# Performance work log

Hardware: AMD Instinct MI355X
Metric: run time of the kernel (lower is better)

Reference implementation:

```python
import jax, jax.numpy as jnp
import numpy as np

LN_EPS = 1e-5   # torch nn.LayerNorm default
EPS = 1e-3      # module eps for norm denominator


def setup_inputs() -> dict:
    key = jax.random.key(0)
    ks = jax.random.split(key, 4)
    N_msa, N_tok, c_m, c_h, c_z = 64, 384, 64, 32, 128
    m = jax.random.normal(ks[0], (N_msa, N_tok, c_m), dtype=jnp.float32)
    mask = jnp.ones((N_msa, N_tok), dtype=jnp.float32)
    ln_w = jnp.ones((c_m,), dtype=jnp.float32)
    ln_b = jnp.zeros((c_m,), dtype=jnp.float32)
    w1 = jax.random.normal(ks[1], (c_h, c_m), dtype=jnp.float32) * (1.0 / np.sqrt(c_m))
    w2 = jax.random.normal(ks[2], (c_h, c_m), dtype=jnp.float32) * (1.0 / np.sqrt(c_m))
    w_out = jax.random.normal(ks[3], (c_z, c_h * c_h), dtype=jnp.float32) * (1.0 / np.sqrt(c_h * c_h))
    b_out = jnp.zeros((c_z,), dtype=jnp.float32)
    return {"m": m, "mask": mask, "ln_w": ln_w, "ln_b": ln_b,
            "w1": w1, "w2": w2, "w_out": w_out, "b_out": b_out}


def reference(m, mask, ln_w, ln_b, w1, w2, w_out, b_out):
    # LayerNorm over c_m
    mu = jnp.mean(m, axis=-1, keepdims=True)
    var = jnp.var(m, axis=-1, keepdims=True)
    m_n = (m - mu) * jax.lax.rsqrt(var + LN_EPS) * ln_w + ln_b

    maskx = mask[..., None]                                   # (N_msa, N_tok, 1)
    # norm[i,j] = sum_s mask[s,i]*mask[s,j], shape (N_tok, N_tok, 1)
    norm = jnp.einsum('sic,sjc->ijc', maskx, maskx)

    a = jnp.einsum('sim,cm->sic', m_n, w1) * maskx            # (N_msa, N_tok, C)
    b = jnp.einsum('sim,cm->sic', m_n, w2) * maskx            # (N_msa, N_tok, C)

    # mean-of-outer-products over MSA rows: (N_tok, N_tok, C, C)
    outer = jnp.einsum('sic,sjd->ijcd', a, b)
    N_tok, C = a.shape[1], a.shape[2]
    outer = outer.reshape(N_tok, N_tok, C * C)

    out = jnp.einsum('ijk,zk->ijz', outer, w_out) + b_out      # (N_tok, N_tok, c_z)
    return out / (norm + EPS)
```

## Files before the change

### kernel.cpp

```cpp
#include <hip/hip_runtime.h>
#include <stdint.h>

#define NS 64
#define NT 384
#define CM 64
#define CH 32
#define CZ 128

typedef __attribute__((ext_vector_type(8))) short bf16x8;
typedef __attribute__((ext_vector_type(16))) float f32x16;
typedef __attribute__((ext_vector_type(4))) float f32x4;
typedef __attribute__((ext_vector_type(4))) uint32_t u32x4;

#define MFMA __builtin_amdgcn_mfma_f32_32x32x16_bf16

static __device__ __forceinline__ uint16_t f2bf(float f) {
  uint32_t u = __float_as_uint(f);
  u = (u + 0x7FFFu + ((u >> 16) & 1u)) >> 16;
  return (uint16_t)u;
}
static __device__ __forceinline__ uint32_t pack2(float lo, float hi) {
  return (uint32_t)f2bf(lo) | ((uint32_t)f2bf(hi) << 16);
}
static __device__ __forceinline__ int swzO(int x) {
  return x ^ ((((x >> 8) ^ (x >> 11)) & 7) << 4);
}

__global__ __launch_bounds__(256) void k_pre(
    const float* __restrict__ m, const float* __restrict__ mask,
    const float* __restrict__ lnw, const float* __restrict__ lnb,
    const float* __restrict__ w1, const float* __restrict__ w2,
    const float* __restrict__ wout,
    uint16_t* __restrict__ AF2, uint16_t* __restrict__ BF,
    uint16_t* __restrict__ W2, float* __restrict__ invn) {
  __shared__ float4 wsh4[2][1024];
  __shared__ float4 mn4[64 * 17];
  const int b = blockIdx.x;
  const int tid = threadIdx.x;
  if (b < NT) {
    const int i = b;
    const int wv = tid >> 6, lane = tid & 63;
    for (int t = tid; t < 1024; t += 256) {
      wsh4[0][t] = ((const float4*)w1)[t];
      wsh4[1][t] = ((const float4*)w2)[t];
    }
    const float lw = lnw[lane], lb = lnb[lane];
    float* mnf = (float*)mn4;
    for (int s = wv; s < NS; s += 4) {
      float x = m[(s * NT + i) * CM + lane];
      float sum = x, sq = x * x;
#pragma unroll
      for (int off = 32; off; off >>= 1) {
        sum += __shfl_xor(sum, off);
        sq += __shfl_xor(sq, off);
      }
      float mu = sum * (1.f / 64.f);
      float var = sq * (1.f / 64.f) - mu * mu;
      float rs = 1.f / sqrtf(var + 1e-5f);
      mnf[s * 68 + lane] = (x - mu) * rs * lw + lb;
    }
    __syncthreads();
    const int s = lane;
    const int cb = tid >> 6;
    float accA[8] = {0, 0, 0, 0, 0, 0, 0, 0};
    float accB[8] = {0, 0, 0, 0, 0, 0, 0, 0};
#pragma unroll
    for (int q = 0; q < 16; ++q) {
      float4 v = mn4[s * 17 + q];
#pragma unroll
      for (int k = 0; k < 8; ++k) {
        float4 wa = wsh4[0][(cb * 8 + k) * 16 + q];
        float4 wb = wsh4[1][(cb * 8 + k) * 16 + q];
        accA[k] = fmaf(v.x, wa.x, fmaf(v.y, wa.y, fmaf(v.z, wa.z, fmaf(v.w, wa.w, accA[k]))));
        accB[k] = fmaf(v.x, wb.x, fmaf(v.y, wb.y, fmaf(v.z, wb.z, fmaf(v.w, wb.w, accB[k]))));
      }
    }
    const float msk = mask[s * NT + i];
    const int kkq = s >> 4, hh = (s >> 3) & 1, e = s & 7;
    const size_t baseB = ((size_t)(i * 4 + kkq) * 64 + hh * 32) * 8 + e;
#pragma unroll
    for (int k = 0; k < 8; ++k) {
      int c = cb * 8 + k;
      BF[baseB + (size_t)c * 8] = f2bf(accB[k] * msk);
      int rb = (c >> 2) * 48 + (i >> 3);
      int r = (i & 7) * 4 + (c & 3);
      AF2[((size_t)(rb * 4 + kkq) * 64 + hh * 32 + r) * 8 + e] = f2bf(accA[k] * msk);
    }
  } else if (b < NT + 64) {
    const int g = (b - NT) * 256 + tid;
    const int l = g & 63, zt = (g >> 6) & 3, kk = g >> 8;
    const float* src = wout + (zt * 32 + (l & 31)) * 1024 + kk * 16 + (l >> 5) * 8;
    uint16_t* dst = W2 + (size_t)g * 8;
#pragma unroll
    for (int e2 = 0; e2 < 8; ++e2) dst[e2] = f2bf(src[e2]);
  } else {
    const int t = (b - NT - 64) * 256 + tid;
    const int i = t / NT, j = t - i * NT;
    float acc = 0.f;
#pragma unroll 8
    for (int s2 = 0; s2 < NS; ++s2) acc += mask[s2 * NT + i] * mask[s2 * NT + j];
    invn[t] = 1.f / (acc + 1e-3f);
  }
}

__global__ __launch_bounds__(512, 2) void k_main(
    const uint16_t* __restrict__ AF2, const uint16_t* __restrict__ BF,
    const uint16_t* __restrict__ W2, const float* __restrict__ b_out,
    const float* __restrict__ invn, float* __restrict__ out) {
  extern __shared__ char lds[];
  const int tid = threadIdx.x;
  const int wv = tid >> 6, l = tid & 63;
  const int lo5 = l & 31, hi = l >> 5;
  const int i0 = blockIdx.x * 16, j0 = blockIdx.y * 8;
  const int ib0 = blockIdx.x * 2;
  const int jt = wv;
  const int kh = wv >> 2, mp = (wv >> 1) & 1, zp = wv & 1;

  bf16x8 bfr[4];
  {
    const uint16_t* p = BF + (size_t)(j0 + jt) * 4 * 512 + (size_t)l * 8;
#pragma unroll
    for (int kk = 0; kk < 4; ++kk) bfr[kk] = *(const bf16x8*)(p + kk * 512);
  }

  f32x16 acc2[2][2];
#pragma unroll
  for (int mi = 0; mi < 2; ++mi)
#pragma unroll
    for (int zi = 0; zi < 2; ++zi) acc2[mi][zi] = (f32x16){};

  for (int cbk = 0; cbk < 8; ++cbk) {
    const int cur = cbk & 1;
    char* ldsO = lds + cur * 32768;
    char* ldsW = lds + 65536 + cur * 32768;

    u32x4 wst[4];
    {
      const uint32_t* src = (const uint32_t*)(W2 + (size_t)cbk * 16384);
#pragma unroll
      for (int it = 0; it < 4; ++it) wst[it] = *(const u32x4*)(src + it * 2048 + tid * 4);
    }

    f32x16 acc1[2];
    acc1[0] = (f32x16){};
    acc1[1] = (f32x16){};
    {
      const uint16_t* Ap = AF2 + (size_t)(cbk * 48 + ib0) * 4 * 512 + (size_t)l * 8;
#pragma unroll
      for (int kk = 0; kk < 4; ++kk) {
        bf16x8 a0 = *(const bf16x8*)(Ap + kk * 512);
        bf16x8 a1 = *(const bf16x8*)(Ap + (4 + kk) * 512);
        acc1[0] = MFMA(bfr[kk], a0, acc1[0], 0, 0, 0);
        acc1[1] = MFMA(bfr[kk], a1, acc1[1], 0, 0, 0);
      }
    }
#pragma unroll
    for (int it = 0; it < 4; ++it) *(u32x4*)(ldsW + it * 8192 + tid * 16) = wst[it];
#pragma unroll
    for (int h = 0; h < 2; ++h) {
      const int p = (h * 8 + (lo5 >> 2)) * 8 + jt;
      const int base = p * 256 + (lo5 & 3) * 64 + hi * 8;
#pragma unroll
      for (int g = 0; g < 4; ++g) {
        uint64_t v = (uint64_t)pack2(acc1[h][4 * g + 0], acc1[h][4 * g + 1]) |
                     ((uint64_t)pack2(acc1[h][4 * g + 2], acc1[h][4 * g + 3]) << 32);
        *(uint64_t*)(ldsO + swzO(base + g * 16)) = v;
      }
    }
    __syncthreads();

#pragma unroll
    for (int kx = 0; kx < 4; ++kx) {
      const int kkl = kh * 4 + kx;
      bf16x8 of[2], wf[2];
#pragma unroll
      for (int mi = 0; mi < 2; ++mi) {
        const int mt = mp * 2 + mi;
        of[mi] = *(const bf16x8*)(ldsO + swzO((mt * 32 + lo5) * 256 + kkl * 32 + hi * 16));
      }
#pragma unroll
      for (int zi = 0; zi < 2; ++zi) {
        const int zt = zp * 2 + zi;
        wf[zi] = *(const bf16x8*)(ldsW + (kkl * 4 + zt) * 1024 + l * 16);
      }
#pragma unroll
      for (int mi = 0; mi < 2; ++mi)
#pragma unroll
        for (int zi = 0; zi < 2; ++zi)
          acc2[mi][zi] = MFMA(of[mi], wf[zi], acc2[mi][zi], 0, 0, 0);
    }
  }

  const int sidx = mp * 2 + zp;
  const int wbase = (sidx < 2) ? sidx * 16384 : 65536 + (sidx - 2) * 16384;
  if (kh == 1) {
#pragma unroll
    for (int mi = 0; mi < 2; ++mi)
#pragma unroll
      for (int zi = 0; zi < 2; ++zi)
#pragma unroll
        for (int g = 0; g < 4; ++g) {
          f32x4 v = {acc2[mi][zi][4 * g + 0], acc2[mi][zi][4 * g + 1],
                     acc2[mi][zi][4 * g + 2], acc2[mi][zi][4 * g + 3]};
          *(f32x4*)(lds + wbase + ((mi * 2 + zi) * 4 + g) * 1024 + l * 16) = v;
        }
  }
  __syncthreads();
  if (kh == 0) {
#pragma unroll
    for (int mi = 0; mi < 2; ++mi)
#pragma unroll
      for (int zi = 0; zi < 2; ++zi)
#pragma unroll
        for (int g = 0; g < 4; ++g) {
          f32x4 v = *(const f32x4*)(lds + wbase + ((mi * 2 + zi) * 4 + g) * 1024 + l * 16);
#pragma unroll
          for (int jj = 0; jj < 4; ++jj) acc2[mi][zi][4 * g + jj] += v[jj];
        }
  }
  if (tid < 128)
    ((float*)(lds + 98304))[tid] = invn[(size_t)(i0 + (tid >> 3)) * NT + j0 + (tid & 7)];
  __syncthreads();
  if (kh == 0) {
    const float bo0 = b_out[(zp * 2) * 32 + lo5];
    const float bo1 = b_out[(zp * 2 + 1) * 32 + lo5];
    const float* invl = (const float*)(lds + 98304);
#pragma unroll
    for (int mi = 0; mi < 2; ++mi) {
      const int mt = mp * 2 + mi;
#pragma unroll
      for (int e = 0; e < 16; ++e) {
        const int row = mt * 32 + (e & 3) + 8 * (e >> 2) + 4 * hi;
        const float inv = invl[row];
        const size_t n = (size_t)(i0 + (row >> 3)) * NT + j0 + (row & 7);
        out[n * CZ + zp * 64 + lo5] = (acc2[mi][0][e] + bo0) * inv;
        out[n * CZ + zp * 64 + 32 + lo5] = (acc2[mi][1][e] + bo1) * inv;
      }
    }
  }
}

extern "C" void kernel_launch(void* const* d_in, const int* in_sizes, int n_in,
                              void* d_out, int out_size, void* d_ws, size_t ws_size,
                              hipStream_t stream) {
  const float* m    = (const float*)d_in[0];
  const float* mask = (const float*)d_in[1];
  const float* lnw  = (const float*)d_in[2];
  const float* lnb  = (const float*)d_in[3];
  const float* w1   = (const float*)d_in[4];
  const float* w2   = (const float*)d_in[5];
  const float* wout = (const float*)d_in[6];
  const float* bout = (const float*)d_in[7];
  float* out = (float*)d_out;

  char* ws = (char*)d_ws;
  uint16_t* AF2 = (uint16_t*)ws;
  uint16_t* BF  = (uint16_t*)(ws + 1572864);
  uint16_t* W2  = (uint16_t*)(ws + 3145728);
  float* invn   = (float*)(ws + 3407872);

  k_pre<<<1024, 256, 0, stream>>>(m, mask, lnw, lnb, w1, w2, wout, AF2, BF, W2, invn);

  (void)hipFuncSetAttribute(reinterpret_cast<const void*>(k_main),
                            hipFuncAttributeMaxDynamicSharedMemorySize, 131072);
  k_main<<<dim3(NT / 16, NT / 8), 512, 131072, stream>>>(AF2, BF, W2, bout, invn, out);
}
```

Measured before the change: 195.1 us.

## Halve k_main tile, read W_out fragments from global, drop split-K reduction

Each block of k_main now covers 8x8 token pairs instead of 16x8, which doubles the grid. The W_out fragments are loaded straight from global/L2 into registers rather than staged through LDS. Each wave owns a full K range for one 32x32 output tile, which removes the cross-wave split-K reduction through LDS. LDS drops to about 33KB static, launch bounds target 4 blocks per CU, and the first-stage product is software-pipelined with one barrier per step. The trade is more repeated global reads of W_out and of the B fragments across the larger grid, in exchange for higher occupancy and less LDS traffic.

```diff
diff --git a/kernel.cpp b/kernel.cpp
--- a/kernel.cpp
+++ b/kernel.cpp
@@ -9,8 +9,6 @@
 
 typedef __attribute__((ext_vector_type(8))) short bf16x8;
 typedef __attribute__((ext_vector_type(16))) float f32x16;
-typedef __attribute__((ext_vector_type(4))) float f32x4;
-typedef __attribute__((ext_vector_type(4))) uint32_t u32x4;
 
 #define MFMA __builtin_amdgcn_mfma_f32_32x32x16_bf16
 
@@ -103,18 +101,21 @@
   }
 }
 
-__global__ __launch_bounds__(512, 2) void k_main(
+__global__ __launch_bounds__(512, 4) void k_main(
     const uint16_t* __restrict__ AF2, const uint16_t* __restrict__ BF,
     const uint16_t* __restrict__ W2, const float* __restrict__ b_out,
     const float* __restrict__ invn, float* __restrict__ out) {
-  extern __shared__ char lds[];
+  __shared__ __align__(16) char lds[2 * 16384 + 256];
+  float* invLds = (float*)(lds + 32768);
   const int tid = threadIdx.x;
   const int wv = tid >> 6, l = tid & 63;
   const int lo5 = l & 31, hi = l >> 5;
-  const int i0 = blockIdx.x * 16, j0 = blockIdx.y * 8;
-  const int ib0 = blockIdx.x * 2;
+  const int ib = blockIdx.x;
+  const int i0 = blockIdx.x * 8, j0 = blockIdx.y * 8;
   const int jt = wv;
-  const int kh = wv >> 2, mp = (wv >> 1) & 1, zp = wv & 1;
+  const int mp = wv >> 2, zp = wv & 3;
+
+  if (tid < 64) invLds[tid] = invn[(size_t)(i0 + (tid >> 3)) * NT + j0 + (tid & 7)];
 
   bf16x8 bfr[4];
   {
@@ -123,120 +124,73 @@
     for (int kk = 0; kk < 4; ++kk) bfr[kk] = *(const bf16x8*)(p + kk * 512);
   }
 
-  f32x16 acc2[2][2];
-#pragma unroll
-  for (int mi = 0; mi < 2; ++mi)
-#pragma unroll
-    for (int zi = 0; zi < 2; ++zi) acc2[mi][zi] = (f32x16){};
-
-  for (int cbk = 0; cbk < 8; ++cbk) {
-    const int cur = cbk & 1;
-    char* ldsO = lds + cur * 32768;
-    char* ldsW = lds + 65536 + cur * 32768;
-
-    u32x4 wst[4];
+  f32x16 acc2 = (f32x16){};
+
+
+  {
+    const uint16_t* Ap = AF2 + ((size_t)(0 * 48 + ib) * 4) * 512 + (size_t)l * 8;
+    f32x16 acc1 = (f32x16){};
+#pragma unroll
+    for (int kk = 0; kk < 4; ++kk) {
+      bf16x8 afr = *(const bf16x8*)(Ap + kk * 512);
+      acc1 = MFMA(bfr[kk], afr, acc1, 0, 0, 0);
+    }
+    const int p = (lo5 >> 2) * 8 + jt;
+    const int base = p * 256 + (lo5 & 3) * 64 + hi * 8;
+#pragma unroll
+    for (int g = 0; g < 4; ++g) {
+      uint64_t v = (uint64_t)pack2(acc1[4 * g + 0], acc1[4 * g + 1]) |
+                   ((uint64_t)pack2(acc1[4 * g + 2], acc1[4 * g + 3]) << 32);
+      *(uint64_t*)(lds + swzO(base + g * 16)) = v;
+    }
+  }
+  __syncthreads();
+
+  const int p2base = (mp * 32 + lo5) * 256 + hi * 16;
+
+  for (int cbk = 1; cbk <= 8; ++cbk) {
+    f32x16 acc1 = (f32x16){};
+    if (cbk < 8) {
+      const uint16_t* Ap = AF2 + ((size_t)(cbk * 48 + ib) * 4) * 512 + (size_t)l * 8;
+#pragma unroll
+      for (int kk = 0; kk < 4; ++kk) {
+        bf16x8 afr = *(const bf16x8*)(Ap + kk * 512);
+        acc1 = MFMA(bfr[kk], afr, acc1, 0, 0, 0);
+      }
+    }
+
     {
-      const uint32_t* src = (const uint32_t*)(W2 + (size_t)cbk * 16384);
-#pragma unroll
-      for (int it = 0; it < 4; ++it) wst[it] = *(const u32x4*)(src + it * 2048 + tid * 4);
-    }
-
-    f32x16 acc1[2];
-    acc1[0] = (f32x16){};
-    acc1[1] = (f32x16){};
-    {
-      const uint16_t* Ap = AF2 + (size_t)(cbk * 48 + ib0) * 4 * 512 + (size_t)l * 8;
-#pragma unroll
-      for (int kk = 0; kk < 4; ++kk) {
-        bf16x8 a0 = *(const bf16x8*)(Ap + kk * 512);
-        bf16x8 a1 = *(const bf16x8*)(Ap + (4 + kk) * 512);
-        acc1[0] = MFMA(bfr[kk], a0, acc1[0], 0, 0, 0);
-        acc1[1] = MFMA(bfr[kk], a1, acc1[1], 0, 0, 0);
-      }
-    }
-#pragma unroll
-    for (int it = 0; it < 4; ++it) *(u32x4*)(ldsW + it * 8192 + tid * 16) = wst[it];
-#pragma unroll
-    for (int h = 0; h < 2; ++h) {
-      const int p = (h * 8 + (lo5 >> 2)) * 8 + jt;
+      char* ldsO = lds + ((cbk - 1) & 1) * 16384;
+      const uint16_t* Wp = W2 + ((size_t)(((cbk - 1) * 8) * 4 + zp) * 64 + l) * 8;
+#pragma unroll
+      for (int kx = 0; kx < 8; ++kx) {
+        bf16x8 of = *(const bf16x8*)(ldsO + swzO(p2base + kx * 32));
+        bf16x8 wf = *(const bf16x8*)(Wp + (size_t)kx * 4 * 512);
+        acc2 = MFMA(of, wf, acc2, 0, 0, 0);
+      }
+    }
+
+    if (cbk < 8) {
+      char* ldsO = lds + (cbk & 1) * 16384;
+      const int p = (lo5 >> 2) * 8 + jt;
       const int base = p * 256 + (lo5 & 3) * 64 + hi * 8;
 #pragma unroll
       for (int g = 0; g < 4; ++g) {
-        uint64_t v = (uint64_t)pack2(acc1[h][4 * g + 0], acc1[h][4 * g + 1]) |
-                     ((uint64_t)pack2(acc1[h][4 * g + 2], acc1[h][4 * g + 3]) << 32);
+        uint64_t v = (uint64_t)pack2(acc1[4 * g + 0], acc1[4 * g + 1]) |
+                     ((uint64_t)pack2(acc1[4 * g + 2], acc1[4 * g + 3]) << 32);
         *(uint64_t*)(ldsO + swzO(base + g * 16)) = v;
       }
-    }
-    __syncthreads();
-
-#pragma unroll
-    for (int kx = 0; kx < 4; ++kx) {
-      const int kkl = kh * 4 + kx;
-      bf16x8 of[2], wf[2];
-#pragma unroll
-      for (int mi = 0; mi < 2; ++mi) {
-        const int mt = mp * 2 + mi;
-        of[mi] = *(const bf16x8*)(ldsO + swzO((mt * 32 + lo5) * 256 + kkl * 32 + hi * 16));
-      }
-#pragma unroll
-      for (int zi = 0; zi < 2; ++zi) {
-        const int zt = zp * 2 + zi;
-        wf[zi] = *(const bf16x8*)(ldsW + (kkl * 4 + zt) * 1024 + l * 16);
-      }
-#pragma unroll
-      for (int mi = 0; mi < 2; ++mi)
-#pragma unroll
-        for (int zi = 0; zi < 2; ++zi)
-          acc2[mi][zi] = MFMA(of[mi], wf[zi], acc2[mi][zi], 0, 0, 0);
-    }
-  }
-
-  const int sidx = mp * 2 + zp;
-  const int wbase = (sidx < 2) ? sidx * 16384 : 65536 + (sidx - 2) * 16384;
-  if (kh == 1) {
-#pragma unroll
-    for (int mi = 0; mi < 2; ++mi)
-#pragma unroll
-      for (int zi = 0; zi < 2; ++zi)
-#pragma unroll
-        for (int g = 0; g < 4; ++g) {
-          f32x4 v = {acc2[mi][zi][4 * g + 0], acc2[mi][zi][4 * g + 1],
-                     acc2[mi][zi][4 * g + 2], acc2[mi][zi][4 * g + 3]};
-          *(f32x4*)(lds + wbase + ((mi * 2 + zi) * 4 + g) * 1024 + l * 16) = v;
-        }
-  }
-  __syncthreads();
-  if (kh == 0) {
-#pragma unroll
-    for (int mi = 0; mi < 2; ++mi)
-#pragma unroll
-      for (int zi = 0; zi < 2; ++zi)
-#pragma unroll
-        for (int g = 0; g < 4; ++g) {
-          f32x4 v = *(const f32x4*)(lds + wbase + ((mi * 2 + zi) * 4 + g) * 1024 + l * 16);
-#pragma unroll
-          for (int jj = 0; jj < 4; ++jj) acc2[mi][zi][4 * g + jj] += v[jj];
-        }
-  }
-  if (tid < 128)
-    ((float*)(lds + 98304))[tid] = invn[(size_t)(i0 + (tid >> 3)) * NT + j0 + (tid & 7)];
-  __syncthreads();
-  if (kh == 0) {
-    const float bo0 = b_out[(zp * 2) * 32 + lo5];
-    const float bo1 = b_out[(zp * 2 + 1) * 32 + lo5];
-    const float* invl = (const float*)(lds + 98304);
-#pragma unroll
-    for (int mi = 0; mi < 2; ++mi) {
-      const int mt = mp * 2 + mi;
-#pragma unroll
-      for (int e = 0; e < 16; ++e) {
-        const int row = mt * 32 + (e & 3) + 8 * (e >> 2) + 4 * hi;
-        const float inv = invl[row];
-        const size_t n = (size_t)(i0 + (row >> 3)) * NT + j0 + (row & 7);
-        out[n * CZ + zp * 64 + lo5] = (acc2[mi][0][e] + bo0) * inv;
-        out[n * CZ + zp * 64 + 32 + lo5] = (acc2[mi][1][e] + bo1) * inv;
-      }
-    }
+      __syncthreads();
+    }
+  }
+
+  const int z = zp * 32 + lo5;
+  const float bo = b_out[z];
+#pragma unroll
+  for (int e = 0; e < 16; ++e) {
+    const int prow = mp * 32 + (e & 3) + 8 * (e >> 2) + 4 * hi;
+    const size_t n = (size_t)(i0 + (prow >> 3)) * NT + j0 + (prow & 7);
+    out[n * CZ + z] = (acc2[e] + bo) * invLds[prow];
   }
 }
 
@@ -260,8 +214,5 @@
   float* invn   = (float*)(ws + 3407872);
 
   k_pre<<<1024, 256, 0, stream>>>(m, mask, lnw, lnb, w1, w2, wout, AF2, BF, W2, invn);
-
-  (void)hipFuncSetAttribute(reinterpret_cast<const void*>(k_main),
-                            hipFuncAttributeMaxDynamicSharedMemorySize, 131072);
-  k_main<<<dim3(NT / 16, NT / 8), 512, 131072, stream>>>(AF2, BF, W2, bout, invn, out);
-}
+  k_main<<<dim3(NT / 8, NT / 8), 512, 0, stream>>>(AF2, BF, W2, bout, invn, out);
+}
```

New measurement: 174.5 us. 10.6% less time.

## Read W_out fragments from global and software-pipeline outer-product stage

Applied to the files above, without the earlier changes.

Stops staging the W_out block in LDS and has each wave read its weight fragments straight from global/L2. The LDS footprint shrinks from 128KB to about 64KB, and launch bounds rise to 4 so more blocks can share a CU. The first outer-product tile is computed before the loop, so tile cbk+1 is built into the alternate LDS buffer while the second GEMM consumes tile cbk. This trades redundant global weight reads per wave for higher occupancy and one fewer LDS write-and-sync pass per iteration.

```diff
diff --git a/kernel.cpp b/kernel.cpp
--- a/kernel.cpp
+++ b/kernel.cpp
@@ -10,7 +10,6 @@
 typedef __attribute__((ext_vector_type(8))) short bf16x8;
 typedef __attribute__((ext_vector_type(16))) float f32x16;
 typedef __attribute__((ext_vector_type(4))) float f32x4;
-typedef __attribute__((ext_vector_type(4))) uint32_t u32x4;
 
 #define MFMA __builtin_amdgcn_mfma_f32_32x32x16_bf16
 
@@ -103,18 +102,21 @@
   }
 }
 
-__global__ __launch_bounds__(512, 2) void k_main(
+__global__ __launch_bounds__(512, 4) void k_main(
     const uint16_t* __restrict__ AF2, const uint16_t* __restrict__ BF,
     const uint16_t* __restrict__ W2, const float* __restrict__ b_out,
     const float* __restrict__ invn, float* __restrict__ out) {
   extern __shared__ char lds[];
+  float* invLds = (float*)(lds + 65536);
   const int tid = threadIdx.x;
   const int wv = tid >> 6, l = tid & 63;
   const int lo5 = l & 31, hi = l >> 5;
+  const int ib0 = blockIdx.x * 2;
   const int i0 = blockIdx.x * 16, j0 = blockIdx.y * 8;
-  const int ib0 = blockIdx.x * 2;
   const int jt = wv;
-  const int kh = wv >> 2, mp = (wv >> 1) & 1, zp = wv & 1;
+  const int kxh = wv >> 2, mp = (wv >> 1) & 1, zp = wv & 1;
+
+  if (tid < 128) invLds[tid] = invn[(size_t)(i0 + (tid >> 3)) * NT + j0 + (tid & 7)];
 
   bf16x8 bfr[4];
   {
@@ -129,71 +131,80 @@
 #pragma unroll
     for (int zi = 0; zi < 2; ++zi) acc2[mi][zi] = (f32x16){};
 
-  for (int cbk = 0; cbk < 8; ++cbk) {
-    const int cur = cbk & 1;
-    char* ldsO = lds + cur * 32768;
-    char* ldsW = lds + 65536 + cur * 32768;
-
-    u32x4 wst[4];
+  const int wcol = (lo5 >> 2) * 8 + jt;
+  const int wbyte = (lo5 & 3) * 64 + hi * 8;
+  const int p2base = mp * 2 * 32 * 256;
+
+  {
+    const uint16_t* Ap = AF2 + ((size_t)(0 * 48 + ib0) * 4) * 512 + (size_t)l * 8;
+#pragma unroll
+    for (int ih = 0; ih < 2; ++ih) {
+      f32x16 a1 = (f32x16){};
+#pragma unroll
+      for (int kk = 0; kk < 4; ++kk) {
+        bf16x8 af = *(const bf16x8*)(Ap + (ih * 4 + kk) * 512);
+        a1 = MFMA(bfr[kk], af, a1, 0, 0, 0);
+      }
+      const int base = (ih * 64 + wcol) * 256 + wbyte;
+#pragma unroll
+      for (int g = 0; g < 4; ++g) {
+        uint64_t v = (uint64_t)pack2(a1[4 * g + 0], a1[4 * g + 1]) |
+                     ((uint64_t)pack2(a1[4 * g + 2], a1[4 * g + 3]) << 32);
+        *(uint64_t*)(lds + swzO(base + g * 16)) = v;
+      }
+    }
+  }
+  __syncthreads();
+
+  for (int cbk = 1; cbk <= 8; ++cbk) {
+    if (cbk < 8) {
+      char* ldsO = lds + (cbk & 1) * 32768;
+      const uint16_t* Ap = AF2 + ((size_t)(cbk * 48 + ib0) * 4) * 512 + (size_t)l * 8;
+#pragma unroll
+      for (int ih = 0; ih < 2; ++ih) {
+        f32x16 a1 = (f32x16){};
+#pragma unroll
+        for (int kk = 0; kk < 4; ++kk) {
+          bf16x8 af = *(const bf16x8*)(Ap + (ih * 4 + kk) * 512);
+          a1 = MFMA(bfr[kk], af, a1, 0, 0, 0);
+        }
+        const int base = (ih * 64 + wcol) * 256 + wbyte;
+#pragma unroll
+        for (int g = 0; g < 4; ++g) {
+          uint64_t v = (uint64_t)pack2(a1[4 * g + 0], a1[4 * g + 1]) |
+                       ((uint64_t)pack2(a1[4 * g + 2], a1[4 * g + 3]) << 32);
+          *(uint64_t*)(ldsO + swzO(base + g * 16)) = v;
+        }
+      }
+    }
+
     {
-      const uint32_t* src = (const uint32_t*)(W2 + (size_t)cbk * 16384);
-#pragma unroll
-      for (int it = 0; it < 4; ++it) wst[it] = *(const u32x4*)(src + it * 2048 + tid * 4);
-    }
-
-    f32x16 acc1[2];
-    acc1[0] = (f32x16){};
-    acc1[1] = (f32x16){};
-    {
-      const uint16_t* Ap = AF2 + (size_t)(cbk * 48 + ib0) * 4 * 512 + (size_t)l * 8;
-#pragma unroll
-      for (int kk = 0; kk < 4; ++kk) {
-        bf16x8 a0 = *(const bf16x8*)(Ap + kk * 512);
-        bf16x8 a1 = *(const bf16x8*)(Ap + (4 + kk) * 512);
-        acc1[0] = MFMA(bfr[kk], a0, acc1[0], 0, 0, 0);
-        acc1[1] = MFMA(bfr[kk], a1, acc1[1], 0, 0, 0);
-      }
-    }
-#pragma unroll
-    for (int it = 0; it < 4; ++it) *(u32x4*)(ldsW + it * 8192 + tid * 16) = wst[it];
-#pragma unroll
-    for (int h = 0; h < 2; ++h) {
-      const int p = (h * 8 + (lo5 >> 2)) * 8 + jt;
-      const int base = p * 256 + (lo5 & 3) * 64 + hi * 8;
-#pragma unroll
-      for (int g = 0; g < 4; ++g) {
-        uint64_t v = (uint64_t)pack2(acc1[h][4 * g + 0], acc1[h][4 * g + 1]) |
-                     ((uint64_t)pack2(acc1[h][4 * g + 2], acc1[h][4 * g + 3]) << 32);
-        *(uint64_t*)(ldsO + swzO(base + g * 16)) = v;
-      }
-    }
-    __syncthreads();
-
-#pragma unroll
-    for (int kx = 0; kx < 4; ++kx) {
-      const int kkl = kh * 4 + kx;
-      bf16x8 of[2], wf[2];
-#pragma unroll
-      for (int mi = 0; mi < 2; ++mi) {
-        const int mt = mp * 2 + mi;
-        of[mi] = *(const bf16x8*)(ldsO + swzO((mt * 32 + lo5) * 256 + kkl * 32 + hi * 16));
-      }
-#pragma unroll
-      for (int zi = 0; zi < 2; ++zi) {
-        const int zt = zp * 2 + zi;
-        wf[zi] = *(const bf16x8*)(ldsW + (kkl * 4 + zt) * 1024 + l * 16);
-      }
-#pragma unroll
-      for (int mi = 0; mi < 2; ++mi)
+      const int t = cbk - 1;
+      char* ldsO = lds + (t & 1) * 32768;
+      const uint16_t* Wp = W2 + ((size_t)((t * 8 + kxh * 4) * 4 + zp * 2) * 64 + l) * 8;
+#pragma unroll
+      for (int kq = 0; kq < 4; ++kq) {
+        const int kx = kxh * 4 + kq;
+        bf16x8 of[2], wf[2];
+#pragma unroll
+        for (int mi = 0; mi < 2; ++mi)
+          of[mi] = *(const bf16x8*)(ldsO + swzO(p2base + mi * 8192 + lo5 * 256 + kx * 32 + hi * 16));
 #pragma unroll
         for (int zi = 0; zi < 2; ++zi)
-          acc2[mi][zi] = MFMA(of[mi], wf[zi], acc2[mi][zi], 0, 0, 0);
-    }
-  }
-
+          wf[zi] = *(const bf16x8*)(Wp + (size_t)(kq * 4 + zi) * 512);
+#pragma unroll
+        for (int mi = 0; mi < 2; ++mi)
+#pragma unroll
+          for (int zi = 0; zi < 2; ++zi)
+            acc2[mi][zi] = MFMA(of[mi], wf[zi], acc2[mi][zi], 0, 0, 0);
+      }
+    }
+    if (cbk < 8) __syncthreads();
+  }
+
+  __syncthreads();
   const int sidx = mp * 2 + zp;
-  const int wbase = (sidx < 2) ? sidx * 16384 : 65536 + (sidx - 2) * 16384;
-  if (kh == 1) {
+  if (kxh == 1) {
 #pragma unroll
     for (int mi = 0; mi < 2; ++mi)
 #pragma unroll
@@ -202,37 +213,31 @@
         for (int g = 0; g < 4; ++g) {
           f32x4 v = {acc2[mi][zi][4 * g + 0], acc2[mi][zi][4 * g + 1],
                      acc2[mi][zi][4 * g + 2], acc2[mi][zi][4 * g + 3]};
-          *(f32x4*)(lds + wbase + ((mi * 2 + zi) * 4 + g) * 1024 + l * 16) = v;
+          *(f32x4*)(lds + sidx * 16384 + ((mi * 2 + zi) * 4 + g) * 1024 + l * 16) = v;
         }
   }
   __syncthreads();
-  if (kh == 0) {
+  if (kxh == 0) {
 #pragma unroll
     for (int mi = 0; mi < 2; ++mi)
 #pragma unroll
       for (int zi = 0; zi < 2; ++zi)
 #pragma unroll
         for (int g = 0; g < 4; ++g) {
-          f32x4 v = *(const f32x4*)(lds + wbase + ((mi * 2 + zi) * 4 + g) * 1024 + l * 16);
+          f32x4 v = *(const f32x4*)(lds + sidx * 16384 + ((mi * 2 + zi) * 4 + g) * 1024 + l * 16);
 #pragma unroll
           for (int jj = 0; jj < 4; ++jj) acc2[mi][zi][4 * g + jj] += v[jj];
         }
-  }
-  if (tid < 128)
-    ((float*)(lds + 98304))[tid] = invn[(size_t)(i0 + (tid >> 3)) * NT + j0 + (tid & 7)];
-  __syncthreads();
-  if (kh == 0) {
     const float bo0 = b_out[(zp * 2) * 32 + lo5];
     const float bo1 = b_out[(zp * 2 + 1) * 32 + lo5];
-    const float* invl = (const float*)(lds + 98304);
 #pragma unroll
     for (int mi = 0; mi < 2; ++mi) {
       const int mt = mp * 2 + mi;
 #pragma unroll
       for (int e = 0; e < 16; ++e) {
-        const int row = mt * 32 + (e & 3) + 8 * (e >> 2) + 4 * hi;
-        const float inv = invl[row];
-        const size_t n = (size_t)(i0 + (row >> 3)) * NT + j0 + (row & 7);
+        const int prow = mt * 32 + (e & 3) + 8 * (e >> 2) + 4 * hi;
+        const float inv = invLds[prow];
+        const size_t n = (size_t)(i0 + (prow >> 3)) * NT + j0 + (prow & 7);
         out[n * CZ + zp * 64 + lo5] = (acc2[mi][0][e] + bo0) * inv;
         out[n * CZ + zp * 64 + 32 + lo5] = (acc2[mi][1][e] + bo1) * inv;
       }
@@ -262,6 +267,6 @@
   k_pre<<<1024, 256, 0, stream>>>(m, mask, lnw, lnb, w1, w2, wout, AF2, BF, W2, invn);
 
   (void)hipFuncSetAttribute(reinterpret_cast<const void*>(k_main),
-                            hipFuncAttributeMaxDynamicSharedMemorySize, 131072);
-  k_main<<<dim3(NT / 16, NT / 8), 512, 131072, stream>>>(AF2, BF, W2, bout, invn, out);
-}
+                            hipFuncAttributeMaxDynamicSharedMemorySize, 66048);
+  k_main<<<dim3(NT / 16, NT / 8), 512, 66048, stream>>>(AF2, BF, W2, bout, invn, out);
+}
```

Measured after the change: 190.5 us. 2.4% less time.
